# Kernel optimization log

Measured on AMD Instinct MI355X. Metric: run time of the kernel, lower is better.

Reference implementation:

```python
import jax, jax.numpy as jnp
import numpy as np

NPOINT = 1024
RADIUS = 0.1
NSAMPLE = 32
EPS = 1e-5


def farthest_point_sample(xyz, npoint):
    # xyz: [B, N, 3] -> indices [B, npoint]
    B, N, _ = xyz.shape

    def step(carry, _):
        mind, far = carry  # [B,N], [B]
        centroid = jnp.take_along_axis(xyz, far[:, None, None], axis=1)  # [B,1,3]
        d = jnp.sum((xyz - centroid) ** 2, axis=-1)  # [B,N]
        mind = jnp.minimum(mind, d)
        return (mind, jnp.argmax(mind, axis=-1).astype(jnp.int32)), far

    init = (jnp.full((B, N), 1e10, xyz.dtype), jnp.zeros((B,), jnp.int32))
    _, idx = jax.lax.scan(step, init, None, length=npoint)  # [npoint, B]
    return idx.T


def ball_query(xyz, new_xyz, radius, nsample):
    # xyz [B,N,3], new_xyz [B,S,3] -> neighbor idx [B,S,nsample]
    N = xyz.shape[1]
    d2 = jnp.sum((new_xyz[:, :, None, :] - xyz[:, None, :, :]) ** 2, axis=-1)  # [B,S,N]
    idx = jnp.where(d2 <= radius ** 2, jnp.arange(N, dtype=jnp.int32), N)
    idx = jnp.sort(idx, axis=-1)[..., :nsample]
    first = idx[..., :1]  # center itself is always in-radius, so first is valid
    return jnp.where(idx == N, first, idx)


def _gather(x, idx):
    # x [B,N,C], idx [B,...] -> [B,...,C]
    return jax.vmap(lambda a, i: a[i])(x, idx)


def setup_inputs() -> dict:
    key = jax.random.key(0)
    ks = jax.random.split(key, 8)
    B, N, D = 16, 8192, 64
    inp = {
        "xyz": jax.random.uniform(ks[0], (B, 3, N), jnp.float32),
        "points": jax.random.normal(ks[1], (B, D, N), jnp.float32),
        "w0": jax.random.normal(ks[2], (64, 67), jnp.float32) * 0.05,
        "b0": jnp.zeros((64,), jnp.float32),
        "g0": jnp.ones((64,), jnp.float32),
        "beta0": jnp.zeros((64,), jnp.float32),
        "w1": jax.random.normal(ks[3], (64, 64), jnp.float32) * 0.05,
        "b1": jnp.zeros((64,), jnp.float32),
        "g1": jnp.ones((64,), jnp.float32),
        "beta1": jnp.zeros((64,), jnp.float32),
        "w2": jax.random.normal(ks[4], (128, 64), jnp.float32) * 0.05,
        "b2": jnp.zeros((128,), jnp.float32),
        "g2": jnp.ones((128,), jnp.float32),
        "beta2": jnp.zeros((128,), jnp.float32),
    }
    return inp


def reference(xyz, points, w0, b0, g0, beta0, w1, b1, g1, beta1, w2, b2, g2, beta2):
    # xyz [B,3,N], points [B,D,N]
    xyz_t = jnp.transpose(xyz, (0, 2, 1))      # [B,N,3]
    pts_t = jnp.transpose(points, (0, 2, 1))   # [B,N,D]

    fps_idx = farthest_point_sample(xyz_t, NPOINT)          # [B,S]
    new_xyz = _gather(xyz_t, fps_idx)                        # [B,S,3]
    gidx = ball_query(xyz_t, new_xyz, RADIUS, NSAMPLE)       # [B,S,K]

    grouped_xyz = _gather(xyz_t, gidx) - new_xyz[:, :, None, :]  # [B,S,K,3]
    grouped_pts = _gather(pts_t, gidx)                           # [B,S,K,D]
    feat = jnp.concatenate([grouped_xyz, grouped_pts], axis=-1)  # [B,S,K,3+D]
    B, S, K, C = feat.shape
    new_points = jnp.transpose(feat.reshape(B, S * K, C), (0, 2, 1))  # [B,C,S*K]

    for w, b, g, be in ((w0, b0, g0, beta0), (w1, b1, g1, beta1), (w2, b2, g2, beta2)):
        x = jnp.einsum('bcl,oc->bol', new_points, w) + b[None, :, None]
        mean = x.mean(axis=(0, 2), keepdims=True)
        var = x.var(axis=(0, 2), keepdims=True)
        new_points = jax.nn.relu(g[None, :, None] * (x - mean)
                                 * jax.lax.rsqrt(var + EPS) + be[None, :, None])

    new_points = jnp.max(new_points, axis=2)  # [B, mlp[-1]]
    return jnp.transpose(new_xyz, (0, 2, 1)), new_points
```

## Files before the change

### kernel.cpp

```cpp
#include <hip/hip_runtime.h>
#include <stdint.h>
#include <limits.h>

__device__ inline float mul_rn(float a, float b){ float r; asm("v_mul_f32 %0, %1, %2" : "=v"(r) : "v"(a), "v"(b)); return r; }
__device__ inline float add_rn(float a, float b){ float r; asm("v_add_f32 %0, %1, %2" : "=v"(r) : "v"(a), "v"(b)); return r; }
__device__ inline float sub_rn(float a, float b){ float r; asm("v_sub_f32 %0, %1, %2" : "=v"(r) : "v"(a), "v"(b)); return r; }

typedef uint16_t u16x8 __attribute__((ext_vector_type(8)));
typedef float    f32x2 __attribute__((ext_vector_type(2)));
typedef short    bf16x8 __attribute__((ext_vector_type(8)));
typedef float    fx4 __attribute__((ext_vector_type(4)));

__device__ inline float bf2f(uint16_t u){ return __uint_as_float(((uint32_t)u) << 16); }
__device__ inline uint16_t f2bf(float f){
    uint32_t u = __float_as_uint(f);
    u += 0x7fffu + ((u >> 16) & 1u);
    return (uint16_t)(u >> 16);
}
__device__ inline unsigned fkey(float f){
    unsigned u = __float_as_uint(f);
    return (u & 0x80000000u) ? ~u : (u | 0x80000000u);
}
__device__ inline float funkey(unsigned k){
    unsigned u = (k & 0x80000000u) ? (k ^ 0x80000000u) : ~k;
    return __uint_as_float(u);
}

__device__ inline unsigned dpp_umax_wave(unsigned v){
    unsigned t;
    t = (unsigned)__builtin_amdgcn_update_dpp((int)v, (int)v, 0x111, 0xf, 0xf, false); v = v > t ? v : t;
    t = (unsigned)__builtin_amdgcn_update_dpp((int)v, (int)v, 0x112, 0xf, 0xf, false); v = v > t ? v : t;
    t = (unsigned)__builtin_amdgcn_update_dpp((int)v, (int)v, 0x114, 0xf, 0xf, false); v = v > t ? v : t;
    t = (unsigned)__builtin_amdgcn_update_dpp((int)v, (int)v, 0x118, 0xf, 0xf, false); v = v > t ? v : t;
    t = (unsigned)__builtin_amdgcn_update_dpp((int)v, (int)v, 0x142, 0xf, 0xf, false); v = v > t ? v : t;
    t = (unsigned)__builtin_amdgcn_update_dpp((int)v, (int)v, 0x143, 0xf, 0xf, false); v = v > t ? v : t;
    return v;
}

#define NPTS   8192
#define NBATCH 16
#define NPOINT 1024
#define NSAMP  32
#define LCOLS  32768
#define NTOT   524288.0f
#define NBUCK  32

#define OFF_FPS   0u
#define OFF_GIDX  65536u
#define OFF_SSC   2162688u
#define OFF_MM    2263040u
#define OFF_WT    2279424u
#define OFF_WPK1  2345728u
#define OFF_WPK2  2353920u
#define OFF_T0    4194304u
#define OFF_T1    71303168u
#define OFF_PTST  138412032u

__global__ __launch_bounds__(512) void fps_fused_kernel(const float* __restrict__ xyz,
        int* __restrict__ fps_idx, float* __restrict__ out_xyz,
        const float* __restrict__ pts, uint16_t* __restrict__ ptsT,
        const float* __restrict__ w0, const float* __restrict__ w1, const float* __restrict__ w2,
        float* __restrict__ wt0, uint16_t* __restrict__ wpk1, uint16_t* __restrict__ wpk2){
#pragma clang fp contract(off)
    __shared__ __align__(16) float smem[33824];
    const int bid = blockIdx.x, tid = threadIdx.x;

    if (bid >= 2064){
        int t = (bid - 2064) * 512 + tid;
        if (t < 64*67){ int o = t / 67, c = t % 67; wt0[c*64 + o] = w0[t]; }
        if (t < 64*64){ int o = t >> 6, c = t & 63; wpk1[((c>>3)*64  + o)*8 + (c&7)] = f2bf(w1[t]); }
        if (t < 128*64){ int o = t >> 6, c = t & 63; wpk2[((c>>3)*128 + o)*8 + (c&7)] = f2bf(w2[t]); }
        return;
    }
    if (bid >= 16){
        float (*tile)[65] = (float(*)[65])smem;
        const int tb = bid - 16;
        const int bt = tb >> 7, n0 = (tb & 127) << 6;
        const int tn = tid & 63, tg = tid >> 6;
        const float* src = pts + (size_t)bt * 64 * NPTS + n0;
#pragma unroll
        for (int i = 0; i < 8; i++){ int c = tg*8 + i; tile[c][tn] = src[(size_t)c * NPTS + tn]; }
        __syncthreads();
        uint16_t* dst = ptsT + ((size_t)bt * NPTS + n0) * 64;
#pragma unroll
        for (int i = 0; i < 8; i++){ int n = tg*8 + i; dst[(size_t)n * 64 + tn] = f2bf(tile[tn][n]); }
        return;
    }

    float* sxyz = smem;
    float4* sxyz4 = (float4*)smem;
    unsigned long long* wslots = (unsigned long long*)(smem + 32768);
    int* sidx = (int*)(smem + 32800);
    const int b = bid;
    const float* px = xyz + (size_t)b * 3 * NPTS;
    for (int i = tid; i < NPTS; i += 512)
        sxyz4[i] = float4{px[i], px[NPTS + i], px[2*NPTS + i], 0.f};
    __syncthreads();

    const int p0 = tid << 4;
    const float4* rp = sxyz4 + p0;
    f32x2 X2[8], Y2[8], Z2[8], M2[8];
#pragma unroll
    for (int j = 0; j < 8; j++){
        float4 qa = rp[2*j], qb = rp[2*j + 1];
        X2[j] = f32x2{qa.x, qb.x};
        Y2[j] = f32x2{qa.y, qb.y};
        Z2[j] = f32x2{qa.z, qb.z};
        M2[j] = f32x2{1e10f, 1e10f};
    }
    const unsigned base = ~(unsigned)p0;

    int cur = 0;
    float cx = sxyz[0], cy = sxyz[1], cz = sxyz[2];
    for (int t = 0; t < NPOINT; t++){
        if (tid == 0) sidx[t] = cur;
        const f32x2 c2x = f32x2{cx, cx}, c2y = f32x2{cy, cy}, c2z = f32x2{cz, cz};
#pragma unroll
        for (int j = 0; j < 8; j++){
            f32x2 dx = X2[j] - c2x;
            f32x2 dy = Y2[j] - c2y;
            f32x2 dz = Z2[j] - c2z;
            f32x2 d2 = dx*dx + dy*dy + dz*dz;
            M2[j].x = fminf(M2[j].x, d2.x);
            M2[j].y = fminf(M2[j].y, d2.y);
        }
        float tv[8];
#pragma unroll
        for (int j = 0; j < 8; j++) tv[j] = fmaxf(M2[j].x, M2[j].y);
        float t0_ = fmaxf(fmaxf(tv[0], tv[1]), fmaxf(tv[2], tv[3]));
        float t1_ = fmaxf(fmaxf(tv[4], tv[5]), fmaxf(tv[6], tv[7]));
        const float mt = fmaxf(t0_, t1_);
        unsigned jpos = 0;
#pragma unroll
        for (int j = 7; j >= 0; j--){
            if (M2[j].y == mt) jpos = 2*j + 1;
            if (M2[j].x == mt) jpos = 2*j;
        }
        const unsigned lo = base - jpos;
        const unsigned mtu = __float_as_uint(mt);
        unsigned vm = dpp_umax_wave(mtu);
        const unsigned wvu = __builtin_amdgcn_readlane(vm, 63);
        unsigned long long cand = __ballot(mtu == wvu);
        const int fl = __ffsll((long long)cand) - 1;
        const unsigned wlo = __builtin_amdgcn_readlane(lo, fl);
        if ((tid & 63) == 0)
            wslots[(t & 1) * 8 + (tid >> 6)] = (((unsigned long long)wvu) << 32) | wlo;
        __syncthreads();
        const ulonglong2* sp = (const ulonglong2*)(wslots + (t & 1) * 8);
        ulonglong2 ka = sp[0], kb = sp[1], kc = sp[2], kd = sp[3];
        unsigned long long ma = (ka.y > ka.x) ? ka.y : ka.x;
        unsigned long long mb = (kb.y > kb.x) ? kb.y : kb.x;
        unsigned long long mc = (kc.y > kc.x) ? kc.y : kc.x;
        unsigned long long md = (kd.y > kd.x) ? kd.y : kd.x;
        unsigned long long mab = (mb > ma) ? mb : ma;
        unsigned long long mcd = (md > mc) ? md : mc;
        unsigned long long win = (mcd > mab) ? mcd : mab;
        cur = (int)(~((unsigned)win));
        const float4 cc4 = sxyz4[cur];
        cx = cc4.x; cy = cc4.y; cz = cc4.z;
    }
    __syncthreads();
#pragma unroll
    for (int q = 0; q < 2; q++){
        const int i = (q << 9) + tid;
        const int idx = sidx[i];
        fps_idx[b * NPOINT + i] = idx;
        const float4 c4 = sxyz4[idx];
        float* oxp = out_xyz + b * 3 * NPOINT;
        oxp[i]            = c4.x;
        oxp[NPOINT + i]   = c4.y;
        oxp[2*NPOINT + i] = c4.z;
    }
}

__global__ __launch_bounds__(256) void ballquery_kernel(const float* __restrict__ xyz,
                                                        const int* __restrict__ fps_idx, int* __restrict__ gidx){
    const int w = (blockIdx.x << 2) + (threadIdx.x >> 6);
    const int lane = threadIdx.x & 63;
    const int b = w >> 10, s = w & 1023;
    const float* px = xyz + (size_t)b * 3 * NPTS;
    const int ci = fps_idx[b * NPOINT + s];
    const float cx = px[ci], cy = px[NPTS+ci], cz = px[2*NPTS+ci];
    int* gout = gidx + (size_t)b * LCOLS + s * NSAMP;
    int have = 0, first_p = 0; bool got = false;
    for (int c0 = 0; c0 < NPTS; c0 += 64){
        int p = c0 + lane;
        float dx = sub_rn(px[p], cx), dy = sub_rn(px[NPTS+p], cy), dz = sub_rn(px[2*NPTS+p], cz);
        float d2 = add_rn(add_rn(mul_rn(dx,dx), mul_rn(dy,dy)), mul_rn(dz,dz));
        bool in = (d2 <= 0.01f);
        unsigned long long m = __ballot(in);
        if (m && !got){ first_p = c0 + __ffsll(m) - 1; got = true; }
        if (in){
            int pos = have + __popcll(m & ((1ull << lane) - 1ull));
            if (pos < NSAMP) gout[pos] = p;
        }
        have += __popcll(m);
        if (have >= NSAMP) break;
    }
    for (int pos = have + lane; pos < NSAMP; pos += 64) gout[pos] = first_p;
}

__global__ __launch_bounds__(256) void mm0_kernel(
        const float* __restrict__ xyz, const float* __restrict__ nx,
        const uint16_t* __restrict__ ptsT, const int* __restrict__ gidx,
        const float* __restrict__ wt, const float* __restrict__ bias,
        uint16_t* __restrict__ xout, float* __restrict__ ssc){
    __shared__ __align__(16) float sw[67 * 64];
    __shared__ float sb[64];
    __shared__ __align__(16) float sred[16 * 260];
    const int tid = threadIdx.x;
    for (int i = tid; i < 67 * 64; i += 256) sw[i] = wt[i];
    if (tid < 64) sb[tid] = bias[tid];
    __syncthreads();
    const int b = blockIdx.x >> 7;
    const int ls = ((blockIdx.x & 127) << 8) + tid;
    float f[67];
    {
        const int s = ls >> 5;
        const int g = gidx[(size_t)b * LCOLS + ls];
        const float* px = xyz + (size_t)b * 3 * NPTS;
        const float cx = nx[b*3*NPOINT + s], cy = nx[b*3*NPOINT + NPOINT + s], cz = nx[b*3*NPOINT + 2*NPOINT + s];
        f[0] = sub_rn(px[g], cx); f[1] = sub_rn(px[NPTS+g], cy); f[2] = sub_rn(px[2*NPTS+g], cz);
        const u16x8* pr = (const u16x8*)(ptsT + ((size_t)b * NPTS + (size_t)g) * 64);
#pragma unroll
        for (int jj = 0; jj < 8; jj++){
            u16x8 v = pr[jj];
#pragma unroll
            for (int e = 0; e < 8; e++) f[3 + jj*8 + e] = bf2f(v[e]);
        }
    }
    uint16_t* op = xout + (size_t)b * 64 * LCOLS + ls;
    float* sbck = ssc + (blockIdx.x & (NBUCK-1)) * 256;
    for (int o0 = 0; o0 < 64; o0 += 16){
        float acc[16];
#pragma unroll
        for (int j = 0; j < 16; j++) acc[j] = sb[o0 + j];
#pragma unroll
        for (int c = 0; c < 67; c++){
            const float4* wr = (const float4*)(sw + c * 64 + o0);
            float4 w0_ = wr[0], w1_ = wr[1], w2_ = wr[2], w3_ = wr[3];
            const float fc = f[c];
            acc[0]  = fmaf(w0_.x, fc, acc[0]);  acc[1]  = fmaf(w0_.y, fc, acc[1]);
            acc[2]  = fmaf(w0_.z, fc, acc[2]);  acc[3]  = fmaf(w0_.w, fc, acc[3]);
            acc[4]  = fmaf(w1_.x, fc, acc[4]);  acc[5]  = fmaf(w1_.y, fc, acc[5]);
            acc[6]  = fmaf(w1_.z, fc, acc[6]);  acc[7]  = fmaf(w1_.w, fc, acc[7]);
            acc[8]  = fmaf(w2_.x, fc, acc[8]);  acc[9]  = fmaf(w2_.y, fc, acc[9]);
            acc[10] = fmaf(w2_.z, fc, acc[10]); acc[11] = fmaf(w2_.w, fc, acc[11]);
            acc[12] = fmaf(w3_.x, fc, acc[12]); acc[13] = fmaf(w3_.y, fc, acc[13]);
            acc[14] = fmaf(w3_.z, fc, acc[14]); acc[15] = fmaf(w3_.w, fc, acc[15]);
        }
#pragma unroll
        for (int j = 0; j < 16; j++) op[(size_t)(o0 + j) * LCOLS] = f2bf(acc[j]);
        __syncthreads();
#pragma unroll
        for (int k = 0; k < 16; k++) sred[k * 260 + tid] = acc[k];
        __syncthreads();
        const int ch = tid >> 4, seg = tid & 15;
        float s = 0.f, ss = 0.f;
        const float4* rp = (const float4*)(sred + ch * 260 + seg * 16);
#pragma unroll
        for (int e = 0; e < 4; e++){
            float4 v = rp[e];
            s += v.x + v.y + v.z + v.w;
            ss = fmaf(v.x, v.x, ss); ss = fmaf(v.y, v.y, ss);
            ss = fmaf(v.z, v.z, ss); ss = fmaf(v.w, v.w, ss);
        }
#pragma unroll
        for (int off = 1; off < 16; off <<= 1){
            s += __shfl_xor(s, off); ss += __shfl_xor(ss, off);
        }
        if (seg == 0){
            atomicAdd(&sbck[o0 + ch], s);
            atomicAdd(&sbck[128 + o0 + ch], ss);
        }
    }
}

template<int COUT, bool WRITE, bool MAXMIN>
__global__ __launch_bounds__(256) void mfma_mm_kernel(
        const uint16_t* __restrict__ xin, const uint16_t* __restrict__ wpack,
        const float* __restrict__ bias,
        const float* __restrict__ pssc, const float* __restrict__ pg, const float* __restrict__ pbeta,
        uint16_t* __restrict__ xout, float* __restrict__ ssc,
        unsigned* __restrict__ mmax, unsigned* __restrict__ mmin){
    constexpr int MT = COUT / 16;
    __shared__ __align__(16) uint16_t sB[8 * 256 * 8];
    __shared__ __align__(16) uint16_t sA[8 * COUT * 8];
    __shared__ float sa_[64], sc_[64], sb_[COUT];
    __shared__ float sred_s[4][COUT], sred_ss[4][COUT];
    __shared__ float sred_mx[MAXMIN ? 4 : 1][COUT], sred_mn[MAXMIN ? 4 : 1][COUT];
    const int tid = threadIdx.x;
    const int b = blockIdx.x >> 7;
    const int n0 = (blockIdx.x & 127) << 8;

    if (tid < 64){
        float s = 0.f, ss = 0.f;
#pragma unroll 4
        for (int k = 0; k < NBUCK; k++){ s += pssc[k*256 + tid]; ss += pssc[k*256 + 128 + tid]; }
        const float inv = 1.0f / NTOT;
        float mean = s * inv;
        float var  = ss * inv - mean * mean;
        float a = pg[tid] / sqrtf(var + 1e-5f);
        sa_[tid] = a;
        sc_[tid] = fmaf(-mean, a, pbeta[tid]);
    }
    if (tid < COUT) sb_[tid] = bias[tid];
    for (int i = tid; i < COUT * 64; i += 256) sA[i] = wpack[i];
    __syncthreads();

    {
        const uint16_t* xp = xin + (size_t)b * 64 * LCOLS + (n0 + tid);
#pragma unroll 8
        for (int c = 0; c < 64; c++){
            float v = bf2f(xp[(size_t)c * LCOLS]);
            v = fmaxf(fmaf(sa_[c], v, sc_[c]), 0.0f);
            sB[((c >> 3) * 256 + tid) * 8 + (c & 7)] = f2bf(v);
        }
    }
    __syncthreads();

    const int lane = tid & 63, w = tid >> 6;
    const int lhi = lane >> 4, llo = lane & 15;
    fx4 acc[MT][4];
#pragma unroll
    for (int mt = 0; mt < MT; mt++)
#pragma unroll
        for (int nt = 0; nt < 4; nt++) acc[mt][nt] = fx4{0.f, 0.f, 0.f, 0.f};

#pragma unroll
    for (int kk = 0; kk < 2; kk++){
        bf16x8 bfrag[4];
#pragma unroll
        for (int nt = 0; nt < 4; nt++){
            int n = w * 64 + nt * 16 + llo;
            bfrag[nt] = *(const bf16x8*)&sB[((kk*4 + lhi) * 256 + n) * 8];
        }
#pragma unroll
        for (int mt = 0; mt < MT; mt++){
            bf16x8 afrag = *(const bf16x8*)&sA[((kk*4 + lhi) * COUT + mt*16 + llo) * 8];
#pragma unroll
            for (int nt = 0; nt < 4; nt++)
                acc[mt][nt] = __builtin_amdgcn_mfma_f32_16x16x32_bf16(afrag, bfrag[nt], acc[mt][nt], 0, 0, 0);
        }
    }

#pragma unroll
    for (int mt = 0; mt < MT; mt++){
#pragma unroll
        for (int j = 0; j < 4; j++){
            const int ch = mt*16 + lhi*4 + j;
            const float bv = sb_[ch];
            float a0 = acc[mt][0][j] + bv, a1 = acc[mt][1][j] + bv;
            float a2 = acc[mt][2][j] + bv, a3 = acc[mt][3][j] + bv;
            acc[mt][0][j] = a0; acc[mt][1][j] = a1; acc[mt][2][j] = a2; acc[mt][3][j] = a3;
            if constexpr (WRITE){
                uint16_t* op = xout + (size_t)b * COUT * LCOLS + (size_t)ch * LCOLS + n0 + w*64 + llo;
                op[0]  = f2bf(a0); op[16] = f2bf(a1); op[32] = f2bf(a2); op[48] = f2bf(a3);
            }
            float s  = (a0 + a1) + (a2 + a3);
            float ss = fmaf(a0, a0, fmaf(a1, a1, fmaf(a2, a2, a3*a3)));
            float mx = 0.f, mn = 0.f;
            if constexpr (MAXMIN){
                mx = fmaxf(fmaxf(a0, a1), fmaxf(a2, a3));
                mn = fminf(fminf(a0, a1), fminf(a2, a3));
            }
#pragma unroll
            for (int off = 1; off < 16; off <<= 1){
                s += __shfl_xor(s, off); ss += __shfl_xor(ss, off);
                if constexpr (MAXMIN){ mx = fmaxf(mx, __shfl_xor(mx, off)); mn = fminf(mn, __shfl_xor(mn, off)); }
            }
            if (llo == 0){
                sred_s[w][ch] = s; sred_ss[w][ch] = ss;
                if constexpr (MAXMIN){ sred_mx[w][ch] = mx; sred_mn[w][ch] = mn; }
            }
        }
    }
    __syncthreads();
    if (tid < COUT){
        float s  = sred_s[0][tid]  + sred_s[1][tid]  + sred_s[2][tid]  + sred_s[3][tid];
        float ss = sred_ss[0][tid] + sred_ss[1][tid] + sred_ss[2][tid] + sred_ss[3][tid];
        float* sbck = ssc + (blockIdx.x & (NBUCK-1)) * 256;
        atomicAdd(&sbck[tid], s);
        atomicAdd(&sbck[128 + tid], ss);
        if constexpr (MAXMIN){
            float mx = fmaxf(fmaxf(sred_mx[0][tid], sred_mx[1][tid]), fmaxf(sred_mx[2][tid], sred_mx[3][tid]));
            float mn = fminf(fminf(sred_mn[0][tid], sred_mn[1][tid]), fminf(sred_mn[2][tid], sred_mn[3][tid]));
            atomicMax(&mmax[b * 128 + tid], fkey(mx));
            atomicMin(&mmin[b * 128 + tid], fkey(mn));
        }
    }
}

__global__ __launch_bounds__(64) void final_kernel(const float* __restrict__ ssc, const float* __restrict__ g2,
                                                   const float* __restrict__ be2, const unsigned* __restrict__ mmax,
                                                   const unsigned* __restrict__ mmin, float* __restrict__ out){
    const int t = blockIdx.x * 64 + threadIdx.x;
    const int o = t & 127;
    float s = 0.f, ss = 0.f;
    for (int k = 0; k < NBUCK; k++){ s += ssc[k*256 + o]; ss += ssc[k*256 + 128 + o]; }
    const float inv = 1.0f / NTOT;
    float mean = s * inv;
    float var  = ss * inv - mean * mean;
    float a = g2[o] / sqrtf(var + 1e-5f);
    float c = fmaf(-mean, a, be2[o]);
    unsigned k = (a >= 0.f) ? mmax[t] : mmin[t];
    float x = funkey(k);
    out[49152 + t] = fmaxf(fmaf(a, x, c), 0.0f);
}

extern "C" void kernel_launch(void* const* d_in, const int* in_sizes, int n_in,
                              void* d_out, int out_size, void* d_ws, size_t ws_size,
                              hipStream_t stream){
    const float* xyz = (const float*)d_in[0];
    const float* pts = (const float*)d_in[1];
    const float* w0  = (const float*)d_in[2];  const float* b0  = (const float*)d_in[3];
    const float* g0  = (const float*)d_in[4];  const float* be0 = (const float*)d_in[5];
    const float* w1  = (const float*)d_in[6];  const float* b1  = (const float*)d_in[7];
    const float* g1  = (const float*)d_in[8];  const float* be1 = (const float*)d_in[9];
    const float* w2  = (const float*)d_in[10]; const float* b2  = (const float*)d_in[11];
    const float* g2  = (const float*)d_in[12]; const float* be2 = (const float*)d_in[13];
    float* out = (float*)d_out;
    char* ws = (char*)d_ws;

    int*      fps_idx = (int*)(ws + OFF_FPS);
    int*      gidx    = (int*)(ws + OFF_GIDX);
    float*    ssc0    = (float*)(ws + OFF_SSC);
    float*    ssc1    = ssc0 + NBUCK*256;
    float*    ssc2    = ssc1 + NBUCK*256;
    unsigned* mmax    = (unsigned*)(ws + OFF_MM);
    unsigned* mmin    = mmax + 2048;
    float*    wt0     = (float*)(ws + OFF_WT);
    uint16_t* wpk1    = (uint16_t*)(ws + OFF_WPK1);
    uint16_t* wpk2    = (uint16_t*)(ws + OFF_WPK2);
    uint16_t* t0      = (uint16_t*)(ws + OFF_T0);
    uint16_t* t1      = (uint16_t*)(ws + OFF_T1);
    uint16_t* ptsT    = (uint16_t*)(ws + OFF_PTST);

    hipMemsetAsync(ws + OFF_SSC, 0, 3 * NBUCK * 256 * 4, stream);
    hipMemsetAsync(ws + OFF_MM, 0x00, 8192, stream);
    hipMemsetAsync(ws + OFF_MM + 8192, 0xFF, 8192, stream);

    fps_fused_kernel<<<2080, 512, 0, stream>>>(xyz, fps_idx, out, pts, ptsT,
                                               w0, w1, w2, wt0, wpk1, wpk2);
    ballquery_kernel<<<4096, 256, 0, stream>>>(xyz, fps_idx, gidx);

    mm0_kernel<<<2048, 256, 0, stream>>>(xyz, out, ptsT, gidx, wt0, b0, t0, ssc0);

    mfma_mm_kernel<64, true, false><<<2048, 256, 0, stream>>>(
        t0, wpk1, b1, ssc0, g0, be0, t1, ssc1, nullptr, nullptr);

    mfma_mm_kernel<128, false, true><<<2048, 256, 0, stream>>>(
        t1, wpk2, b2, ssc1, g1, be1, nullptr, ssc2, mmax, mmin);

    final_kernel<<<32, 64, 0, stream>>>(ssc2, g2, be2, mmax, mmin, out);
}
```

Measured before the change: 1.214 ms.

## Move layer-0 matmul to MFMA and recompute layer-1 instead of storing it

Layer 0 now runs on bf16 MFMA instead of a scalar FP32 FMA loop. Its weights are packed with K padded to 96 and the xyz channels placed after the point features. Layer 1's output is no longer written to memory: one pass computes only layer-1 statistics, and a fused kernel then recomputes layer 1 from t0 and feeds layer 2 through shared memory. This trades extra MFMA work for removing the t1 write and read. It also adds bf16 rounding of the xyz offsets and the layer-0 inputs, which slightly changes numerics.

```diff
diff --git a/kernel.cpp b/kernel.cpp
--- a/kernel.cpp
+++ b/kernel.cpp
@@ -49,25 +49,30 @@
 #define OFF_GIDX  65536u
 #define OFF_SSC   2162688u
 #define OFF_MM    2263040u
-#define OFF_WT    2279424u
-#define OFF_WPK1  2345728u
-#define OFF_WPK2  2353920u
+#define OFF_WPK0  2279424u
+#define OFF_WPK1  2291712u
+#define OFF_WPK2  2299904u
 #define OFF_T0    4194304u
-#define OFF_T1    71303168u
 #define OFF_PTST  138412032u
 
 __global__ __launch_bounds__(512) void fps_fused_kernel(const float* __restrict__ xyz,
         int* __restrict__ fps_idx, float* __restrict__ out_xyz,
         const float* __restrict__ pts, uint16_t* __restrict__ ptsT,
         const float* __restrict__ w0, const float* __restrict__ w1, const float* __restrict__ w2,
-        float* __restrict__ wt0, uint16_t* __restrict__ wpk1, uint16_t* __restrict__ wpk2){
+        uint16_t* __restrict__ wpk0, uint16_t* __restrict__ wpk1, uint16_t* __restrict__ wpk2){
 #pragma clang fp contract(off)
     __shared__ __align__(16) float smem[33824];
     const int bid = blockIdx.x, tid = threadIdx.x;
 
     if (bid >= 2064){
         int t = (bid - 2064) * 512 + tid;
-        if (t < 64*67){ int o = t / 67, c = t % 67; wt0[c*64 + o] = w0[t]; }
+        if (t < 64*96){
+            int o = t / 96, cp = t % 96;
+            uint16_t v = 0;
+            if (cp < 64)      v = f2bf(w0[o*67 + (cp + 3)]);
+            else if (cp < 67) v = f2bf(w0[o*67 + (cp - 64)]);
+            wpk0[((cp>>3)*64 + o)*8 + (cp&7)] = v;
+        }
         if (t < 64*64){ int o = t >> 6, c = t & 63; wpk1[((c>>3)*64  + o)*8 + (c&7)] = f2bf(w1[t]); }
         if (t < 128*64){ int o = t >> 6, c = t & 63; wpk2[((c>>3)*128 + o)*8 + (c&7)] = f2bf(w2[t]); }
         return;
@@ -200,95 +205,102 @@
     for (int pos = have + lane; pos < NSAMP; pos += 64) gout[pos] = first_p;
 }
 
-__global__ __launch_bounds__(256) void mm0_kernel(
+__global__ __launch_bounds__(256) void mfma_mm0_kernel(
         const float* __restrict__ xyz, const float* __restrict__ nx,
         const uint16_t* __restrict__ ptsT, const int* __restrict__ gidx,
-        const float* __restrict__ wt, const float* __restrict__ bias,
+        const uint16_t* __restrict__ wpack, const float* __restrict__ bias,
         uint16_t* __restrict__ xout, float* __restrict__ ssc){
-    __shared__ __align__(16) float sw[67 * 64];
-    __shared__ float sb[64];
-    __shared__ __align__(16) float sred[16 * 260];
+    __shared__ __align__(16) uint16_t sB[12 * 256 * 8];
+    __shared__ __align__(16) uint16_t sA[12 * 64 * 8];
+    __shared__ float sb_[64];
+    __shared__ float sred_s[4][64], sred_ss[4][64];
     const int tid = threadIdx.x;
-    for (int i = tid; i < 67 * 64; i += 256) sw[i] = wt[i];
-    if (tid < 64) sb[tid] = bias[tid];
-    __syncthreads();
     const int b = blockIdx.x >> 7;
-    const int ls = ((blockIdx.x & 127) << 8) + tid;
-    float f[67];
+    const int n0 = (blockIdx.x & 127) << 8;
+
+    if (tid < 64) sb_[tid] = bias[tid];
+    for (int i = tid; i < 12*64; i += 256) *(u16x8*)&sA[i*8] = *(const u16x8*)&wpack[i*8];
+    __syncthreads();
     {
+        const int ls = n0 + tid;
         const int s = ls >> 5;
         const int g = gidx[(size_t)b * LCOLS + ls];
         const float* px = xyz + (size_t)b * 3 * NPTS;
-        const float cx = nx[b*3*NPOINT + s], cy = nx[b*3*NPOINT + NPOINT + s], cz = nx[b*3*NPOINT + 2*NPOINT + s];
-        f[0] = sub_rn(px[g], cx); f[1] = sub_rn(px[NPTS+g], cy); f[2] = sub_rn(px[2*NPTS+g], cz);
+        float f0 = sub_rn(px[g],        nx[b*3*NPOINT + s]);
+        float f1 = sub_rn(px[NPTS+g],   nx[b*3*NPOINT + NPOINT + s]);
+        float f2 = sub_rn(px[2*NPTS+g], nx[b*3*NPOINT + 2*NPOINT + s]);
         const u16x8* pr = (const u16x8*)(ptsT + ((size_t)b * NPTS + (size_t)g) * 64);
 #pragma unroll
-        for (int jj = 0; jj < 8; jj++){
-            u16x8 v = pr[jj];
-#pragma unroll
-            for (int e = 0; e < 8; e++) f[3 + jj*8 + e] = bf2f(v[e]);
-        }
-    }
-    uint16_t* op = xout + (size_t)b * 64 * LCOLS + ls;
-    float* sbck = ssc + (blockIdx.x & (NBUCK-1)) * 256;
-    for (int o0 = 0; o0 < 64; o0 += 16){
-        float acc[16];
-#pragma unroll
-        for (int j = 0; j < 16; j++) acc[j] = sb[o0 + j];
-#pragma unroll
-        for (int c = 0; c < 67; c++){
-            const float4* wr = (const float4*)(sw + c * 64 + o0);
-            float4 w0_ = wr[0], w1_ = wr[1], w2_ = wr[2], w3_ = wr[3];
-            const float fc = f[c];
-            acc[0]  = fmaf(w0_.x, fc, acc[0]);  acc[1]  = fmaf(w0_.y, fc, acc[1]);
-            acc[2]  = fmaf(w0_.z, fc, acc[2]);  acc[3]  = fmaf(w0_.w, fc, acc[3]);
-            acc[4]  = fmaf(w1_.x, fc, acc[4]);  acc[5]  = fmaf(w1_.y, fc, acc[5]);
-            acc[6]  = fmaf(w1_.z, fc, acc[6]);  acc[7]  = fmaf(w1_.w, fc, acc[7]);
-            acc[8]  = fmaf(w2_.x, fc, acc[8]);  acc[9]  = fmaf(w2_.y, fc, acc[9]);
-            acc[10] = fmaf(w2_.z, fc, acc[10]); acc[11] = fmaf(w2_.w, fc, acc[11]);
-            acc[12] = fmaf(w3_.x, fc, acc[12]); acc[13] = fmaf(w3_.y, fc, acc[13]);
-            acc[14] = fmaf(w3_.z, fc, acc[14]); acc[15] = fmaf(w3_.w, fc, acc[15]);
-        }
-#pragma unroll
-        for (int j = 0; j < 16; j++) op[(size_t)(o0 + j) * LCOLS] = f2bf(acc[j]);
-        __syncthreads();
-#pragma unroll
-        for (int k = 0; k < 16; k++) sred[k * 260 + tid] = acc[k];
-        __syncthreads();
-        const int ch = tid >> 4, seg = tid & 15;
-        float s = 0.f, ss = 0.f;
-        const float4* rp = (const float4*)(sred + ch * 260 + seg * 16);
-#pragma unroll
-        for (int e = 0; e < 4; e++){
-            float4 v = rp[e];
-            s += v.x + v.y + v.z + v.w;
-            ss = fmaf(v.x, v.x, ss); ss = fmaf(v.y, v.y, ss);
-            ss = fmaf(v.z, v.z, ss); ss = fmaf(v.w, v.w, ss);
-        }
-#pragma unroll
-        for (int off = 1; off < 16; off <<= 1){
-            s += __shfl_xor(s, off); ss += __shfl_xor(ss, off);
-        }
-        if (seg == 0){
-            atomicAdd(&sbck[o0 + ch], s);
-            atomicAdd(&sbck[128 + o0 + ch], ss);
-        }
-    }
-}
-
-template<int COUT, bool WRITE, bool MAXMIN>
-__global__ __launch_bounds__(256) void mfma_mm_kernel(
+        for (int kc = 0; kc < 8; kc++) *(u16x8*)&sB[(kc*256 + tid)*8] = pr[kc];
+        u16x8 xrow; xrow[0] = f2bf(f0); xrow[1] = f2bf(f1); xrow[2] = f2bf(f2);
+        xrow[3] = 0; xrow[4] = 0; xrow[5] = 0; xrow[6] = 0; xrow[7] = 0;
+        *(u16x8*)&sB[(8*256 + tid)*8] = xrow;
+        u16x8 zr; zr[0]=0;zr[1]=0;zr[2]=0;zr[3]=0;zr[4]=0;zr[5]=0;zr[6]=0;zr[7]=0;
+#pragma unroll
+        for (int kc = 9; kc < 12; kc++) *(u16x8*)&sB[(kc*256 + tid)*8] = zr;
+    }
+    __syncthreads();
+
+    const int lane = tid & 63, w = tid >> 6;
+    const int lhi = lane >> 4, llo = lane & 15;
+    fx4 acc[4][4];
+#pragma unroll
+    for (int mt = 0; mt < 4; mt++)
+#pragma unroll
+        for (int nt = 0; nt < 4; nt++) acc[mt][nt] = fx4{0.f,0.f,0.f,0.f};
+
+#pragma unroll
+    for (int kk = 0; kk < 3; kk++){
+        bf16x8 bfrag[4];
+#pragma unroll
+        for (int nt = 0; nt < 4; nt++){
+            int n = w * 64 + nt * 16 + llo;
+            bfrag[nt] = *(const bf16x8*)&sB[((kk*4 + lhi) * 256 + n) * 8];
+        }
+#pragma unroll
+        for (int mt = 0; mt < 4; mt++){
+            bf16x8 afrag = *(const bf16x8*)&sA[((kk*4 + lhi) * 64 + mt*16 + llo) * 8];
+#pragma unroll
+            for (int nt = 0; nt < 4; nt++)
+                acc[mt][nt] = __builtin_amdgcn_mfma_f32_16x16x32_bf16(afrag, bfrag[nt], acc[mt][nt], 0, 0, 0);
+        }
+    }
+#pragma unroll
+    for (int mt = 0; mt < 4; mt++){
+#pragma unroll
+        for (int j = 0; j < 4; j++){
+            const int ch = mt*16 + lhi*4 + j;
+            const float bv = sb_[ch];
+            float a0 = acc[mt][0][j] + bv, a1 = acc[mt][1][j] + bv;
+            float a2 = acc[mt][2][j] + bv, a3 = acc[mt][3][j] + bv;
+            uint16_t* op = xout + (size_t)b * 64 * LCOLS + (size_t)ch * LCOLS + n0 + w*64 + llo;
+            op[0]  = f2bf(a0); op[16] = f2bf(a1); op[32] = f2bf(a2); op[48] = f2bf(a3);
+            float s  = (a0 + a1) + (a2 + a3);
+            float ss = fmaf(a0, a0, fmaf(a1, a1, fmaf(a2, a2, a3*a3)));
+#pragma unroll
+            for (int off = 1; off < 16; off <<= 1){ s += __shfl_xor(s, off); ss += __shfl_xor(ss, off); }
+            if (llo == 0){ sred_s[w][ch] = s; sred_ss[w][ch] = ss; }
+        }
+    }
+    __syncthreads();
+    if (tid < 64){
+        float s  = sred_s[0][tid]  + sred_s[1][tid]  + sred_s[2][tid]  + sred_s[3][tid];
+        float ss = sred_ss[0][tid] + sred_ss[1][tid] + sred_ss[2][tid] + sred_ss[3][tid];
+        float* sbck = ssc + (blockIdx.x & (NBUCK-1)) * 256;
+        atomicAdd(&sbck[tid], s);
+        atomicAdd(&sbck[128 + tid], ss);
+    }
+}
+
+__global__ __launch_bounds__(256) void mfma_stats1_kernel(
         const uint16_t* __restrict__ xin, const uint16_t* __restrict__ wpack,
         const float* __restrict__ bias,
         const float* __restrict__ pssc, const float* __restrict__ pg, const float* __restrict__ pbeta,
-        uint16_t* __restrict__ xout, float* __restrict__ ssc,
-        unsigned* __restrict__ mmax, unsigned* __restrict__ mmin){
-    constexpr int MT = COUT / 16;
+        float* __restrict__ ssc){
     __shared__ __align__(16) uint16_t sB[8 * 256 * 8];
-    __shared__ __align__(16) uint16_t sA[8 * COUT * 8];
-    __shared__ float sa_[64], sc_[64], sb_[COUT];
-    __shared__ float sred_s[4][COUT], sred_ss[4][COUT];
-    __shared__ float sred_mx[MAXMIN ? 4 : 1][COUT], sred_mn[MAXMIN ? 4 : 1][COUT];
+    __shared__ __align__(16) uint16_t sA[8 * 64 * 8];
+    __shared__ float sa_[64], sc_[64], sb_[64];
+    __shared__ float sred_s[4][64], sred_ss[4][64];
     const int tid = threadIdx.x;
     const int b = blockIdx.x >> 7;
     const int n0 = (blockIdx.x & 127) << 8;
@@ -303,11 +315,10 @@
         float a = pg[tid] / sqrtf(var + 1e-5f);
         sa_[tid] = a;
         sc_[tid] = fmaf(-mean, a, pbeta[tid]);
-    }
-    if (tid < COUT) sb_[tid] = bias[tid];
-    for (int i = tid; i < COUT * 64; i += 256) sA[i] = wpack[i];
-    __syncthreads();
-
+        sb_[tid] = bias[tid];
+    }
+    for (int i = tid; i < 64*8; i += 256) *(u16x8*)&sA[i*8] = *(const u16x8*)&wpack[i*8];
+    __syncthreads();
     {
         const uint16_t* xp = xin + (size_t)b * 64 * LCOLS + (n0 + tid);
 #pragma unroll 8
@@ -318,15 +329,13 @@
         }
     }
     __syncthreads();
-
     const int lane = tid & 63, w = tid >> 6;
     const int lhi = lane >> 4, llo = lane & 15;
-    fx4 acc[MT][4];
-#pragma unroll
-    for (int mt = 0; mt < MT; mt++)
-#pragma unroll
-        for (int nt = 0; nt < 4; nt++) acc[mt][nt] = fx4{0.f, 0.f, 0.f, 0.f};
-
+    fx4 acc[4][4];
+#pragma unroll
+    for (int mt = 0; mt < 4; mt++)
+#pragma unroll
+        for (int nt = 0; nt < 4; nt++) acc[mt][nt] = fx4{0.f,0.f,0.f,0.f};
 #pragma unroll
     for (int kk = 0; kk < 2; kk++){
         bf16x8 bfrag[4];
@@ -336,58 +345,178 @@
             bfrag[nt] = *(const bf16x8*)&sB[((kk*4 + lhi) * 256 + n) * 8];
         }
 #pragma unroll
-        for (int mt = 0; mt < MT; mt++){
-            bf16x8 afrag = *(const bf16x8*)&sA[((kk*4 + lhi) * COUT + mt*16 + llo) * 8];
+        for (int mt = 0; mt < 4; mt++){
+            bf16x8 afrag = *(const bf16x8*)&sA[((kk*4 + lhi) * 64 + mt*16 + llo) * 8];
 #pragma unroll
             for (int nt = 0; nt < 4; nt++)
                 acc[mt][nt] = __builtin_amdgcn_mfma_f32_16x16x32_bf16(afrag, bfrag[nt], acc[mt][nt], 0, 0, 0);
         }
     }
-
-#pragma unroll
-    for (int mt = 0; mt < MT; mt++){
+#pragma unroll
+    for (int mt = 0; mt < 4; mt++){
 #pragma unroll
         for (int j = 0; j < 4; j++){
             const int ch = mt*16 + lhi*4 + j;
             const float bv = sb_[ch];
             float a0 = acc[mt][0][j] + bv, a1 = acc[mt][1][j] + bv;
             float a2 = acc[mt][2][j] + bv, a3 = acc[mt][3][j] + bv;
-            acc[mt][0][j] = a0; acc[mt][1][j] = a1; acc[mt][2][j] = a2; acc[mt][3][j] = a3;
-            if constexpr (WRITE){
-                uint16_t* op = xout + (size_t)b * COUT * LCOLS + (size_t)ch * LCOLS + n0 + w*64 + llo;
-                op[0]  = f2bf(a0); op[16] = f2bf(a1); op[32] = f2bf(a2); op[48] = f2bf(a3);
-            }
             float s  = (a0 + a1) + (a2 + a3);
             float ss = fmaf(a0, a0, fmaf(a1, a1, fmaf(a2, a2, a3*a3)));
-            float mx = 0.f, mn = 0.f;
-            if constexpr (MAXMIN){
-                mx = fmaxf(fmaxf(a0, a1), fmaxf(a2, a3));
-                mn = fminf(fminf(a0, a1), fminf(a2, a3));
-            }
-#pragma unroll
-            for (int off = 1; off < 16; off <<= 1){
-                s += __shfl_xor(s, off); ss += __shfl_xor(ss, off);
-                if constexpr (MAXMIN){ mx = fmaxf(mx, __shfl_xor(mx, off)); mn = fminf(mn, __shfl_xor(mn, off)); }
-            }
-            if (llo == 0){
-                sred_s[w][ch] = s; sred_ss[w][ch] = ss;
-                if constexpr (MAXMIN){ sred_mx[w][ch] = mx; sred_mn[w][ch] = mn; }
-            }
-        }
-    }
-    __syncthreads();
-    if (tid < COUT){
+#pragma unroll
+            for (int off = 1; off < 16; off <<= 1){ s += __shfl_xor(s, off); ss += __shfl_xor(ss, off); }
+            if (llo == 0){ sred_s[w][ch] = s; sred_ss[w][ch] = ss; }
+        }
+    }
+    __syncthreads();
+    if (tid < 64){
         float s  = sred_s[0][tid]  + sred_s[1][tid]  + sred_s[2][tid]  + sred_s[3][tid];
         float ss = sred_ss[0][tid] + sred_ss[1][tid] + sred_ss[2][tid] + sred_ss[3][tid];
         float* sbck = ssc + (blockIdx.x & (NBUCK-1)) * 256;
         atomicAdd(&sbck[tid], s);
         atomicAdd(&sbck[128 + tid], ss);
-        if constexpr (MAXMIN){
-            float mx = fmaxf(fmaxf(sred_mx[0][tid], sred_mx[1][tid]), fmaxf(sred_mx[2][tid], sred_mx[3][tid]));
-            float mn = fminf(fminf(sred_mn[0][tid], sred_mn[1][tid]), fminf(sred_mn[2][tid], sred_mn[3][tid]));
-            atomicMax(&mmax[b * 128 + tid], fkey(mx));
-            atomicMin(&mmin[b * 128 + tid], fkey(mn));
-        }
+    }
+}
+
+__global__ __launch_bounds__(256) void mfma_mm12_kernel(
+        const uint16_t* __restrict__ xin,
+        const uint16_t* __restrict__ wpk1, const uint16_t* __restrict__ wpk2,
+        const float* __restrict__ b1, const float* __restrict__ b2,
+        const float* __restrict__ ssc0, const float* __restrict__ g0, const float* __restrict__ be0,
+        const float* __restrict__ ssc1, const float* __restrict__ g1, const float* __restrict__ be1,
+        float* __restrict__ ssc2, unsigned* __restrict__ mmax, unsigned* __restrict__ mmin){
+    __shared__ __align__(16) uint16_t sB[8 * 256 * 8];
+    __shared__ __align__(16) uint16_t sA1[8 * 64 * 8];
+    __shared__ __align__(16) uint16_t sA2[8 * 128 * 8];
+    __shared__ float sa0_[64], sc0_[64], sa1_[64], sc1_[64], sb1_[64], sb2_[128];
+    __shared__ float sred_s[4][128], sred_ss[4][128], sred_mx[4][128], sred_mn[4][128];
+    const int tid = threadIdx.x;
+    const int b = blockIdx.x >> 7;
+    const int n0 = (blockIdx.x & 127) << 8;
+
+    if (tid < 64){
+        float s0 = 0.f, ss0 = 0.f, s1 = 0.f, ss1 = 0.f;
+#pragma unroll 4
+        for (int k = 0; k < NBUCK; k++){
+            s0 += ssc0[k*256 + tid]; ss0 += ssc0[k*256 + 128 + tid];
+            s1 += ssc1[k*256 + tid]; ss1 += ssc1[k*256 + 128 + tid];
+        }
+        const float inv = 1.0f / NTOT;
+        float m0 = s0 * inv, v0 = ss0 * inv - m0*m0;
+        float a0 = g0[tid] / sqrtf(v0 + 1e-5f);
+        sa0_[tid] = a0; sc0_[tid] = fmaf(-m0, a0, be0[tid]);
+        float m1 = s1 * inv, v1 = ss1 * inv - m1*m1;
+        float a1 = g1[tid] / sqrtf(v1 + 1e-5f);
+        sa1_[tid] = a1; sc1_[tid] = fmaf(-m1, a1, be1[tid]);
+        sb1_[tid] = b1[tid];
+    }
+    if (tid < 128) sb2_[tid] = b2[tid];
+    for (int i = tid; i < 64*8; i += 256)  *(u16x8*)&sA1[i*8] = *(const u16x8*)&wpk1[i*8];
+    for (int i = tid; i < 128*8; i += 256) *(u16x8*)&sA2[i*8] = *(const u16x8*)&wpk2[i*8];
+    __syncthreads();
+    {
+        const uint16_t* xp = xin + (size_t)b * 64 * LCOLS + (n0 + tid);
+#pragma unroll 8
+        for (int c = 0; c < 64; c++){
+            float v = bf2f(xp[(size_t)c * LCOLS]);
+            v = fmaxf(fmaf(sa0_[c], v, sc0_[c]), 0.0f);
+            sB[((c >> 3) * 256 + tid) * 8 + (c & 7)] = f2bf(v);
+        }
+    }
+    __syncthreads();
+    const int lane = tid & 63, w = tid >> 6;
+    const int lhi = lane >> 4, llo = lane & 15;
+
+    fx4 acc1[4][4];
+#pragma unroll
+    for (int mt = 0; mt < 4; mt++)
+#pragma unroll
+        for (int nt = 0; nt < 4; nt++) acc1[mt][nt] = fx4{0.f,0.f,0.f,0.f};
+#pragma unroll
+    for (int kk = 0; kk < 2; kk++){
+        bf16x8 bfrag[4];
+#pragma unroll
+        for (int nt = 0; nt < 4; nt++){
+            int n = w * 64 + nt * 16 + llo;
+            bfrag[nt] = *(const bf16x8*)&sB[((kk*4 + lhi) * 256 + n) * 8];
+        }
+#pragma unroll
+        for (int mt = 0; mt < 4; mt++){
+            bf16x8 afrag = *(const bf16x8*)&sA1[((kk*4 + lhi) * 64 + mt*16 + llo) * 8];
+#pragma unroll
+            for (int nt = 0; nt < 4; nt++)
+                acc1[mt][nt] = __builtin_amdgcn_mfma_f32_16x16x32_bf16(afrag, bfrag[nt], acc1[mt][nt], 0, 0, 0);
+        }
+    }
+    __syncthreads();
+
+#pragma unroll
+    for (int mt = 0; mt < 4; mt++){
+#pragma unroll
+        for (int j = 0; j < 4; j++){
+            const int ch = mt*16 + lhi*4 + j;
+            const float bv = sb1_[ch], av = sa1_[ch], cv = sc1_[ch];
+#pragma unroll
+            for (int nt = 0; nt < 4; nt++){
+                float z = fmaxf(fmaf(av, acc1[mt][nt][j] + bv, cv), 0.0f);
+                int n = w*64 + nt*16 + llo;
+                sB[((ch >> 3) * 256 + n) * 8 + (ch & 7)] = f2bf(z);
+            }
+        }
+    }
+    __syncthreads();
+
+    fx4 acc2[8][4];
+#pragma unroll
+    for (int mt = 0; mt < 8; mt++)
+#pragma unroll
+        for (int nt = 0; nt < 4; nt++) acc2[mt][nt] = fx4{0.f,0.f,0.f,0.f};
+#pragma unroll
+    for (int kk = 0; kk < 2; kk++){
+        bf16x8 bfrag[4];
+#pragma unroll
+        for (int nt = 0; nt < 4; nt++){
+            int n = w * 64 + nt * 16 + llo;
+            bfrag[nt] = *(const bf16x8*)&sB[((kk*4 + lhi) * 256 + n) * 8];
+        }
+#pragma unroll
+        for (int mt = 0; mt < 8; mt++){
+            bf16x8 afrag = *(const bf16x8*)&sA2[((kk*4 + lhi) * 128 + mt*16 + llo) * 8];
+#pragma unroll
+            for (int nt = 0; nt < 4; nt++)
+                acc2[mt][nt] = __builtin_amdgcn_mfma_f32_16x16x32_bf16(afrag, bfrag[nt], acc2[mt][nt], 0, 0, 0);
+        }
+    }
+#pragma unroll
+    for (int mt = 0; mt < 8; mt++){
+#pragma unroll
+        for (int j = 0; j < 4; j++){
+            const int ch = mt*16 + lhi*4 + j;
+            const float bv = sb2_[ch];
+            float a0 = acc2[mt][0][j] + bv, a1 = acc2[mt][1][j] + bv;
+            float a2 = acc2[mt][2][j] + bv, a3 = acc2[mt][3][j] + bv;
+            float s  = (a0 + a1) + (a2 + a3);
+            float ss = fmaf(a0, a0, fmaf(a1, a1, fmaf(a2, a2, a3*a3)));
+            float mx = fmaxf(fmaxf(a0, a1), fmaxf(a2, a3));
+            float mn = fminf(fminf(a0, a1), fminf(a2, a3));
+#pragma unroll
+            for (int off = 1; off < 16; off <<= 1){
+                s += __shfl_xor(s, off); ss += __shfl_xor(ss, off);
+                mx = fmaxf(mx, __shfl_xor(mx, off)); mn = fminf(mn, __shfl_xor(mn, off));
+            }
+            if (llo == 0){ sred_s[w][ch] = s; sred_ss[w][ch] = ss; sred_mx[w][ch] = mx; sred_mn[w][ch] = mn; }
+        }
+    }
+    __syncthreads();
+    if (tid < 128){
+        float s  = sred_s[0][tid]  + sred_s[1][tid]  + sred_s[2][tid]  + sred_s[3][tid];
+        float ss = sred_ss[0][tid] + sred_ss[1][tid] + sred_ss[2][tid] + sred_ss[3][tid];
+        float mx = fmaxf(fmaxf(sred_mx[0][tid], sred_mx[1][tid]), fmaxf(sred_mx[2][tid], sred_mx[3][tid]));
+        float mn = fminf(fminf(sred_mn[0][tid], sred_mn[1][tid]), fminf(sred_mn[2][tid], sred_mn[3][tid]));
+        float* sbck = ssc2 + (blockIdx.x & (NBUCK-1)) * 256;
+        atomicAdd(&sbck[tid], s);
+        atomicAdd(&sbck[128 + tid], ss);
+        atomicMax(&mmax[b * 128 + tid], fkey(mx));
+        atomicMin(&mmin[b * 128 + tid], fkey(mn));
     }
 }
 
@@ -429,11 +558,10 @@
     float*    ssc2    = ssc1 + NBUCK*256;
     unsigned* mmax    = (unsigned*)(ws + OFF_MM);
     unsigned* mmin    = mmax + 2048;
-    float*    wt0     = (float*)(ws + OFF_WT);
+    uint16_t* wpk0    = (uint16_t*)(ws + OFF_WPK0);
     uint16_t* wpk1    = (uint16_t*)(ws + OFF_WPK1);
     uint16_t* wpk2    = (uint16_t*)(ws + OFF_WPK2);
     uint16_t* t0      = (uint16_t*)(ws + OFF_T0);
-    uint16_t* t1      = (uint16_t*)(ws + OFF_T1);
     uint16_t* ptsT    = (uint16_t*)(ws + OFF_PTST);
 
     hipMemsetAsync(ws + OFF_SSC, 0, 3 * NBUCK * 256 * 4, stream);
@@ -441,16 +569,16 @@
     hipMemsetAsync(ws + OFF_MM + 8192, 0xFF, 8192, stream);
 
     fps_fused_kernel<<<2080, 512, 0, stream>>>(xyz, fps_idx, out, pts, ptsT,
-                                               w0, w1, w2, wt0, wpk1, wpk2);
+                                               w0, w1, w2, wpk0, wpk1, wpk2);
     ballquery_kernel<<<4096, 256, 0, stream>>>(xyz, fps_idx, gidx);
 
-    mm0_kernel<<<2048, 256, 0, stream>>>(xyz, out, ptsT, gidx, wt0, b0, t0, ssc0);
-
-    mfma_mm_kernel<64, true, false><<<2048, 256, 0, stream>>>(
-        t0, wpk1, b1, ssc0, g0, be0, t1, ssc1, nullptr, nullptr);
-
-    mfma_mm_kernel<128, false, true><<<2048, 256, 0, stream>>>(
-        t1, wpk2, b2, ssc1, g1, be1, nullptr, ssc2, mmax, mmin);
+    mfma_mm0_kernel<<<2048, 256, 0, stream>>>(xyz, out, ptsT, gidx, wpk0, b0, t0, ssc0);
+
+    mfma_stats1_kernel<<<2048, 256, 0, stream>>>(t0, wpk1, b1, ssc0, g0, be0, ssc1);
+
+    mfma_mm12_kernel<<<2048, 256, 0, stream>>>(t0, wpk1, wpk2, b1, b2,
+                                               ssc0, g0, be0, ssc1, g1, be1,
+                                               ssc2, mmax, mmin);
 
     final_kernel<<<32, 64, 0, stream>>>(ssc2, g2, be2, mmax, mmin, out);
 }
```

Result: no change. 1.223 ms (+0.7%).
